# Performance work log

Measured on AMD Instinct MI355X. Metric: run time of the kernel, lower is better.

Reference implementation:

```python
import jax, jax.numpy as jnp
import numpy as np

NEG_SLOPE = 0.2
NUM_HEADS = 8
HEAD_DIM = 16


def setup_inputs() -> dict:
    key = jax.random.key(0)
    ks = jax.random.split(key, 14)
    n_nodes, n_edges = 50000, 800000
    in_f, out_f, e_f, H, D = 256, 128, 64, NUM_HEADS, HEAD_DIM
    s = lambda fan_in: 1.0 / np.sqrt(fan_in)
    return {
        "node_features": jax.random.normal(ks[0], (n_nodes, in_f), jnp.float32),
        "edge_index": jax.random.randint(ks[1], (2, n_edges), 0, n_nodes),
        "edge_features": jax.random.normal(ks[2], (n_edges, e_f), jnp.float32),
        "Wl": jax.random.normal(ks[3], (in_f, out_f), jnp.float32) * s(in_f),
        "bl": jnp.zeros((out_f,), jnp.float32),
        "Wr": jax.random.normal(ks[4], (in_f, out_f), jnp.float32) * s(in_f),
        "br": jnp.zeros((out_f,), jnp.float32),
        "We": jax.random.normal(ks[5], (e_f, H), jnp.float32) * s(e_f),
        "be": jnp.zeros((H,), jnp.float32),
        "attn_vector": jax.random.normal(ks[6], (H, D), jnp.float32) * 0.01,
        "Wv": jax.random.normal(ks[7], (in_f, out_f), jnp.float32) * s(in_f),
        "bv": jnp.zeros((out_f,), jnp.float32),
        "Wo": jax.random.normal(ks[8], (out_f, out_f), jnp.float32) * s(out_f),
        "bo": jnp.zeros((out_f,), jnp.float32),
    }


def reference(node_features, edge_index, edge_features,
              Wl, bl, Wr, br, We, be, attn_vector, Wv, bv, Wo, bo):
    n_nodes = node_features.shape[0]
    n_edges = edge_index.shape[1]
    H, D = attn_vector.shape
    sources, targets = edge_index[0], edge_index[1]

    # node projections: [N, H, D]
    left = (node_features @ Wl + bl).reshape(n_nodes, H, D)
    right = (node_features @ Wr + br).reshape(n_nodes, H, D)

    # per-edge GATv2 score: a^T LeakyReLU(W_l h_t + W_r h_s) + edge bias
    combined = left[targets] + right[sources]                      # [E, H, D]
    activated = jax.nn.leaky_relu(combined, negative_slope=NEG_SLOPE)
    attn_scores = jnp.einsum("ehd,hd->eh", activated, attn_vector)  # [E, H]
    attn_scores = attn_scores + (edge_features @ We + be)

    # segment softmax over incoming edges per target node
    max_scores = jax.ops.segment_max(attn_scores, targets, num_segments=n_nodes)
    attn_exp = jnp.exp(attn_scores - max_scores[targets])
    attn_sum = jax.ops.segment_sum(attn_exp, targets, num_segments=n_nodes) + 1e-10
    attn_probs = attn_exp / attn_sum[targets]                      # [E, H]

    # weighted scatter-aggregate of values
    values = (node_features @ Wv + bv).reshape(n_nodes, H, D)
    weighted = attn_probs[:, :, None] * values[sources]            # [E, H, D]
    aggregated = jax.ops.segment_sum(
        weighted.reshape(n_edges, H * D), targets, num_segments=n_nodes)
    return aggregated @ Wo + bo
```

## Files before the change

### kernel.cpp

```cpp
#include <hip/hip_runtime.h>
#include <hip/hip_bf16.h>
#include <stdint.h>

#define NUM_H 8
#define DIM 16
#define HD 128
#define IN_F 256
#define E_F 64
#define NEG_SLOPE 0.2f
#define NB 8
#define EB 32

#define NCT 24
#define KSTEPS 8
#define WELEMS (KSTEPS * NCT * 64 * 8)

typedef __bf16 bf16x8 __attribute__((ext_vector_type(8)));
typedef float f32x4 __attribute__((ext_vector_type(4)));
typedef short short8 __attribute__((ext_vector_type(8)));

__device__ __forceinline__ float b2f(__hip_bfloat16 x) { return __bfloat162float(x); }
__device__ __forceinline__ __hip_bfloat16 f2b(float x) { return __float2bfloat16(x); }
__device__ __forceinline__ float bs2f(short s) {
    uint32_t u = ((uint32_t)(uint16_t)s) << 16;
    return __builtin_bit_cast(float, u);
}

__global__ void k_zero_int(int* p, int n) {
    int i = blockIdx.x * blockDim.x + threadIdx.x;
    int stride = gridDim.x * blockDim.x;
    for (; i < n; i += stride) p[i] = 0;
}

__global__ void k_hist(const int* __restrict__ eidx, int* __restrict__ deg, int n_edges) {
    int e = blockIdx.x * blockDim.x + threadIdx.x;
    if (e < n_edges) atomicAdd(&deg[eidx[n_edges + e]], 1);
}

__global__ void k_scan(const int* __restrict__ deg, int* __restrict__ offs,
                       int* __restrict__ cursor, int n) {
    __shared__ int part[1024];
    int tid = threadIdx.x;
    int chunk = (n + 1023) / 1024;
    int base = tid * chunk;
    int hi = base + chunk < n ? base + chunk : n;
    int sum = 0;
    for (int i = base; i < hi; i++) sum += deg[i];
    part[tid] = sum;
    __syncthreads();
    for (int off = 1; off < 1024; off <<= 1) {
        int v = (tid >= off) ? part[tid - off] : 0;
        __syncthreads();
        part[tid] += v;
        __syncthreads();
    }
    int run = (tid == 0) ? 0 : part[tid - 1];
    for (int i = base; i < hi; i++) {
        offs[i] = run;
        cursor[i] = run;
        run += deg[i];
    }
    if (tid == 0) offs[n] = part[1023];
}

__global__ void k_scatter(const int* __restrict__ eidx, int* __restrict__ cursor,
                          int* __restrict__ eid, int n_edges) {
    int e = blockIdx.x * blockDim.x + threadIdx.x;
    if (e >= n_edges) return;
    int t = eidx[n_edges + e];
    int pos = atomicAdd(&cursor[t], 1);
    eid[pos] = e;
}

__global__ void k_wprep(const float* __restrict__ Wl, const float* __restrict__ Wr,
                        const float* __restrict__ Wv,
                        __bf16* __restrict__ Whi, __bf16* __restrict__ Wlo) {
    int tid = blockIdx.x * blockDim.x + threadIdx.x;
    if (tid >= KSTEPS * NCT * 64) return;
    int l = tid & 63;
    int ctks = tid >> 6;
    int ct = ctks % NCT;
    int ks = ctks / NCT;
    int gc = ct * 16 + (l & 15);
    int m = gc >> 7;
    int c = gc & 127;
    const float* W = (m == 0) ? Wl : (m == 1) ? Wr : Wv;
    bf16x8 h8, l8;
#pragma unroll
    for (int i = 0; i < 8; i++) {
        int k = ks * 32 + ((l >> 4) << 3) + i;
        float w = W[k * HD + c];
        __bf16 hi = (__bf16)w;
        __bf16 lo = (__bf16)(w - (float)hi);
        h8[i] = hi;
        l8[i] = lo;
    }
    *(bf16x8*)(Whi + (size_t)tid * 8) = h8;
    *(bf16x8*)(Wlo + (size_t)tid * 8) = l8;
}

__global__ __launch_bounds__(256, 2) void k_projm(
    const float* __restrict__ nf,
    const __bf16* __restrict__ Whi, const __bf16* __restrict__ Wlo,
    const float* __restrict__ bl, const float* __restrict__ br,
    const float* __restrict__ bv,
    __hip_bfloat16* __restrict__ left, __hip_bfloat16* __restrict__ right,
    __hip_bfloat16* __restrict__ val, int n_nodes) {
    int l = threadIdx.x & 63;
    int wave = threadIdx.x >> 6;
    int row0 = blockIdx.x * 64 + wave * 16;
    if (row0 >= n_nodes) return;
    int lr = l & 15, lg = l >> 4;
    const float* arow = nf + (size_t)(row0 + lr) * IN_F + lg * 8;

    const f32x4 zero = {0.f, 0.f, 0.f, 0.f};
    f32x4 acc[NCT];
#pragma unroll
    for (int ct = 0; ct < NCT; ct++) acc[ct] = zero;

    for (int ks = 0; ks < KSTEPS; ks++) {
        f32x4 a0 = *(const f32x4*)(arow + ks * 32);
        f32x4 a1 = *(const f32x4*)(arow + ks * 32 + 4);
        bf16x8 ah, al;
#pragma unroll
        for (int i = 0; i < 4; i++) {
            __bf16 h = (__bf16)a0[i];
            ah[i] = h;
            al[i] = (__bf16)(a0[i] - (float)h);
        }
#pragma unroll
        for (int i = 0; i < 4; i++) {
            __bf16 h = (__bf16)a1[i];
            ah[4 + i] = h;
            al[4 + i] = (__bf16)(a1[i] - (float)h);
        }
        const bf16x8* wh = (const bf16x8*)(Whi) + (size_t)ks * NCT * 64 + l;
        const bf16x8* wl = (const bf16x8*)(Wlo) + (size_t)ks * NCT * 64 + l;
#pragma unroll
        for (int ct = 0; ct < NCT; ct++) {
            bf16x8 bh = wh[ct * 64];
            bf16x8 blo = wl[ct * 64];
            acc[ct] = __builtin_amdgcn_mfma_f32_16x16x32_bf16(ah, bh, acc[ct], 0, 0, 0);
            acc[ct] = __builtin_amdgcn_mfma_f32_16x16x32_bf16(al, bh, acc[ct], 0, 0, 0);
            acc[ct] = __builtin_amdgcn_mfma_f32_16x16x32_bf16(ah, blo, acc[ct], 0, 0, 0);
        }
    }

#pragma unroll
    for (int ct = 0; ct < NCT; ct++) {
        const int m = ct >> 3;
        int c = ((ct & 7) << 4) + lr;
        float bias = (m == 0) ? bl[c] : (m == 1) ? br[c] : bv[c];
        __hip_bfloat16* dst = (m == 0) ? left : (m == 1) ? right : val;
#pragma unroll
        for (int r = 0; r < 4; r++) {
            int row = row0 + lg * 4 + r;
            dst[(size_t)row * HD + c] = f2b(acc[ct][r] + bias);
        }
    }
}

__global__ __launch_bounds__(256) void k_escore(
    const int* __restrict__ eidx, const float* __restrict__ ef,
    const float* __restrict__ We, const float* __restrict__ be,
    const float* __restrict__ av,
    const __hip_bfloat16* __restrict__ left,
    const __hip_bfloat16* __restrict__ right,
    __hip_bfloat16* __restrict__ es, int n_edges) {
    __shared__ float sef[EB][68];
    int tid = threadIdx.x;
    int e0 = blockIdx.x * EB;
    {
        const f32x4* src = (const f32x4*)(ef + (size_t)e0 * E_F);
        int lim = (n_edges - e0) * (E_F / 4);
        if (lim > EB * (E_F / 4)) lim = EB * (E_F / 4);
#pragma unroll 2
        for (int i = tid; i < lim; i += 256) {
            f32x4 v = src[i];
            int le = i >> 4;
            int k = (i & 15) << 2;
            *(f32x4*)&sef[le][k] = v;
        }
    }
    __syncthreads();
    int le = tid >> 3;
    int h = tid & 7;
    int e = e0 + le;
    if (e >= n_edges) return;
    int s = eidx[e];
    int t = eidx[n_edges + e];

    float sc = be[h];
    const float* row = &sef[le][0];
#pragma unroll
    for (int k4 = 0; k4 < E_F / 4; k4++) {
        f32x4 v = *(const f32x4*)(row + k4 * 4);
        sc += v[0] * We[(k4 * 4 + 0) * NUM_H + h] + v[1] * We[(k4 * 4 + 1) * NUM_H + h] +
              v[2] * We[(k4 * 4 + 2) * NUM_H + h] + v[3] * We[(k4 * 4 + 3) * NUM_H + h];
    }

    const short8* Lp = (const short8*)(left + (size_t)t * HD + h * DIM);
    const short8* Rp = (const short8*)(right + (size_t)s * HD + h * DIM);
    short8 l0 = Lp[0], l1 = Lp[1];
    short8 r0 = Rp[0], r1 = Rp[1];
    const float* avh = av + h * DIM;
#pragma unroll
    for (int d = 0; d < 8; d++) {
        float x = bs2f(l0[d]) + bs2f(r0[d]);
        x = x > 0.0f ? x : NEG_SLOPE * x;
        sc += x * avh[d];
    }
#pragma unroll
    for (int d = 0; d < 8; d++) {
        float x = bs2f(l1[d]) + bs2f(r1[d]);
        x = x > 0.0f ? x : NEG_SLOPE * x;
        sc += x * avh[8 + d];
    }
    es[(size_t)e * NUM_H + h] = f2b(expf(sc));
}

__global__ void k_agg(const int* __restrict__ offs, const int* __restrict__ eid,
                      const int* __restrict__ eidx,
                      const __hip_bfloat16* __restrict__ es,
                      const __hip_bfloat16* __restrict__ val,
                      float* __restrict__ nagg, int n_nodes) {
    int t = blockIdx.x;
    if (t >= n_nodes) return;
    int j = threadIdx.x;
    int h = j >> 4;
    int beg = offs[t], end = offs[t + 1];
    float acc = 0.0f, wsum = 0.0f;
    for (int i = beg; i < end; i++) {
        int e = eid[i];
        int s = eidx[e];
        float w = b2f(es[(size_t)e * NUM_H + h]);
        acc += w * b2f(val[(size_t)s * HD + j]);
        wsum += w;
    }
    nagg[(size_t)t * HD + j] = acc / (wsum + 1e-10f);
}

__global__ void k_out(const float* __restrict__ nagg, const float* __restrict__ Wo,
                      const float* __restrict__ bo, float* __restrict__ out, int n_nodes) {
    __shared__ float srow[NB][HD];
    int node0 = blockIdx.x * NB;
    int j = threadIdx.x;
    for (int i = j; i < NB * HD; i += 128)
        srow[i / HD][i % HD] = nagg[(size_t)node0 * HD + i];
    __syncthreads();
    float a[NB];
    float b = bo[j];
#pragma unroll
    for (int n = 0; n < NB; n++) a[n] = b;
    for (int k = 0; k < HD; k++) {
        float w = Wo[k * HD + j];
#pragma unroll
        for (int n = 0; n < NB; n++) a[n] += srow[n][k] * w;
    }
#pragma unroll
    for (int n = 0; n < NB; n++) out[(size_t)(node0 + n) * HD + j] = a[n];
}

extern "C" void kernel_launch(void* const* d_in, const int* in_sizes, int n_in,
                              void* d_out, int out_size, void* d_ws, size_t ws_size,
                              hipStream_t stream) {
    const float* nf = (const float*)d_in[0];
    const int* eidx = (const int*)d_in[1];
    const float* ef = (const float*)d_in[2];
    const float* Wl = (const float*)d_in[3];
    const float* bl = (const float*)d_in[4];
    const float* Wr = (const float*)d_in[5];
    const float* br = (const float*)d_in[6];
    const float* We = (const float*)d_in[7];
    const float* be = (const float*)d_in[8];
    const float* av = (const float*)d_in[9];
    const float* Wv = (const float*)d_in[10];
    const float* bv = (const float*)d_in[11];
    const float* Wo = (const float*)d_in[12];
    const float* bo = (const float*)d_in[13];
    float* out = (float*)d_out;

    const int n_nodes = in_sizes[0] / IN_F;
    const int n_edges = in_sizes[1] / 2;
    const size_t NHD = (size_t)n_nodes * HD;

    char* base = (char*)d_ws;
    __hip_bfloat16* left  = (__hip_bfloat16*)(base + 256);
    __hip_bfloat16* right = left + NHD;
    __hip_bfloat16* es    = right + NHD;
    int* deg    = (int*)(es + (size_t)n_edges * NUM_H);
    int* offs   = deg + n_nodes;
    int* cursor = offs + n_nodes + 1;
    int* eid    = cursor + n_nodes;
    __bf16* Whi = (__bf16*)es;
    __bf16* Wlo = Whi + (size_t)WELEMS;
    float* nagg = (float*)left;
    __hip_bfloat16* val = (__hip_bfloat16*)d_out;

    int eb = (n_edges + 255) / 256;

    k_wprep<<<(KSTEPS * NCT * 64 + 255) / 256, 256, 0, stream>>>(Wl, Wr, Wv, Whi, Wlo);

    k_zero_int<<<64, 256, 0, stream>>>(deg, n_nodes);
    k_hist<<<eb, 256, 0, stream>>>(eidx, deg, n_edges);
    k_scan<<<1, 1024, 0, stream>>>(deg, offs, cursor, n_nodes);
    k_scatter<<<eb, 256, 0, stream>>>(eidx, cursor, eid, n_edges);

    k_projm<<<(n_nodes + 63) / 64, 256, 0, stream>>>(nf, Whi, Wlo, bl, br, bv,
                                                     left, right, val, n_nodes);

    k_escore<<<(n_edges + EB - 1) / EB, 256, 0, stream>>>(
        eidx, ef, We, be, av, left, right, es, n_edges);

    k_agg<<<n_nodes, 128, 0, stream>>>(offs, eid, eidx, es, val, nagg, n_nodes);

    k_out<<<n_nodes / NB, 128, 0, stream>>>(nagg, Wo, bo, out, n_nodes);
}
```

Measured before the change: 860.7 us.

## Fuse CSR scatter into edge-score kernel and vectorize aggregation per wavefront

The separate scatter kernel is removed. The edge-score kernel now claims a CSR slot per edge with an atomic and writes the exp-score and source index directly in target-sorted order, so aggregation reads them contiguously instead of going through eid and eidx. The aggregation kernel now uses a single 64-lane wavefront per node: it processes four edges at once with 16-byte value loads, then reduces across sub-groups with shuffles. The trade-off is that atomic slot assignment makes the order of floating-point accumulation within each node nondeterministic.

```diff
diff --git a/kernel.cpp b/kernel.cpp
--- a/kernel.cpp
+++ b/kernel.cpp
@@ -63,15 +63,6 @@
     if (tid == 0) offs[n] = part[1023];
 }
 
-__global__ void k_scatter(const int* __restrict__ eidx, int* __restrict__ cursor,
-                          int* __restrict__ eid, int n_edges) {
-    int e = blockIdx.x * blockDim.x + threadIdx.x;
-    if (e >= n_edges) return;
-    int t = eidx[n_edges + e];
-    int pos = atomicAdd(&cursor[t], 1);
-    eid[pos] = e;
-}
-
 __global__ void k_wprep(const float* __restrict__ Wl, const float* __restrict__ Wr,
                         const float* __restrict__ Wv,
                         __bf16* __restrict__ Whi, __bf16* __restrict__ Wlo) {
@@ -166,7 +157,8 @@
     const float* __restrict__ av,
     const __hip_bfloat16* __restrict__ left,
     const __hip_bfloat16* __restrict__ right,
-    __hip_bfloat16* __restrict__ es, int n_edges) {
+    int* __restrict__ cursor, int* __restrict__ srcs,
+    __hip_bfloat16* __restrict__ es_csr, int n_edges) {
     __shared__ float sef[EB][68];
     int tid = threadIdx.x;
     int e0 = blockIdx.x * EB;
@@ -190,6 +182,11 @@
     int s = eidx[e];
     int t = eidx[n_edges + e];
 
+    int lane = tid & 63;
+    int pos = 0;
+    if (h == 0) pos = atomicAdd(&cursor[t], 1);
+    pos = __shfl(pos, lane & ~7);
+
     float sc = be[h];
     const float* row = &sef[le][0];
 #pragma unroll
@@ -216,28 +213,53 @@
         x = x > 0.0f ? x : NEG_SLOPE * x;
         sc += x * avh[8 + d];
     }
-    es[(size_t)e * NUM_H + h] = f2b(expf(sc));
-}
-
-__global__ void k_agg(const int* __restrict__ offs, const int* __restrict__ eid,
-                      const int* __restrict__ eidx,
-                      const __hip_bfloat16* __restrict__ es,
-                      const __hip_bfloat16* __restrict__ val,
-                      float* __restrict__ nagg, int n_nodes) {
+    if (h == 0) srcs[pos] = s;
+    es_csr[(size_t)pos * NUM_H + h] = f2b(expf(sc));
+}
+
+__global__ __launch_bounds__(64) void k_agg(
+    const int* __restrict__ offs, const int* __restrict__ srcs,
+    const __hip_bfloat16* __restrict__ es_csr,
+    const __hip_bfloat16* __restrict__ val,
+    float* __restrict__ nagg, int n_nodes) {
     int t = blockIdx.x;
     if (t >= n_nodes) return;
-    int j = threadIdx.x;
-    int h = j >> 4;
+    int lane = threadIdx.x;
+    int sub = lane >> 4;
+    int c16 = lane & 15;
+    int h = c16 >> 1;
     int beg = offs[t], end = offs[t + 1];
-    float acc = 0.0f, wsum = 0.0f;
-    for (int i = beg; i < end; i++) {
-        int e = eid[i];
-        int s = eidx[e];
-        float w = b2f(es[(size_t)e * NUM_H + h]);
-        acc += w * b2f(val[(size_t)s * HD + j]);
+
+    float acc[8] = {0.f, 0.f, 0.f, 0.f, 0.f, 0.f, 0.f, 0.f};
+    float wsum = 0.0f;
+#pragma unroll 2
+    for (int i0 = beg; i0 < end; i0 += 4) {
+        int i = i0 + sub;
+        bool act = i < end;
+        int ii = act ? i : beg;
+        int s = srcs[ii];
+        float w = b2f(es_csr[(size_t)ii * NUM_H + h]);
+        if (!act) w = 0.0f;
+        short8 v = *(const short8*)(val + (size_t)s * HD + c16 * 8);
         wsum += w;
-    }
-    nagg[(size_t)t * HD + j] = acc / (wsum + 1e-10f);
+#pragma unroll
+        for (int d = 0; d < 8; d++) acc[d] += w * bs2f(v[d]);
+    }
+#pragma unroll
+    for (int m = 16; m <= 32; m <<= 1) {
+        wsum += __shfl_xor(wsum, m);
+#pragma unroll
+        for (int d = 0; d < 8; d++) acc[d] += __shfl_xor(acc[d], m);
+    }
+    if (sub == 0) {
+        float inv = 1.0f / (wsum + 1e-10f);
+        f32x4 o0, o1;
+#pragma unroll
+        for (int d = 0; d < 4; d++) { o0[d] = acc[d] * inv; o1[d] = acc[4 + d] * inv; }
+        float* dst = nagg + (size_t)t * HD + c16 * 8;
+        *(f32x4*)dst = o0;
+        *(f32x4*)(dst + 4) = o1;
+    }
 }
 
 __global__ void k_out(const float* __restrict__ nagg, const float* __restrict__ Wo,
@@ -287,12 +309,12 @@
     char* base = (char*)d_ws;
     __hip_bfloat16* left  = (__hip_bfloat16*)(base + 256);
     __hip_bfloat16* right = left + NHD;
-    __hip_bfloat16* es    = right + NHD;
-    int* deg    = (int*)(es + (size_t)n_edges * NUM_H);
+    __hip_bfloat16* es_csr = right + NHD;
+    int* deg    = (int*)(es_csr + (size_t)n_edges * NUM_H);
     int* offs   = deg + n_nodes;
     int* cursor = offs + n_nodes + 1;
-    int* eid    = cursor + n_nodes;
-    __bf16* Whi = (__bf16*)es;
+    int* srcs   = cursor + n_nodes;
+    __bf16* Whi = (__bf16*)es_csr;
     __bf16* Wlo = Whi + (size_t)WELEMS;
     float* nagg = (float*)left;
     __hip_bfloat16* val = (__hip_bfloat16*)d_out;
@@ -304,15 +326,14 @@
     k_zero_int<<<64, 256, 0, stream>>>(deg, n_nodes);
     k_hist<<<eb, 256, 0, stream>>>(eidx, deg, n_edges);
     k_scan<<<1, 1024, 0, stream>>>(deg, offs, cursor, n_nodes);
-    k_scatter<<<eb, 256, 0, stream>>>(eidx, cursor, eid, n_edges);
 
     k_projm<<<(n_nodes + 63) / 64, 256, 0, stream>>>(nf, Whi, Wlo, bl, br, bv,
                                                      left, right, val, n_nodes);
 
     k_escore<<<(n_edges + EB - 1) / EB, 256, 0, stream>>>(
-        eidx, ef, We, be, av, left, right, es, n_edges);
-
-    k_agg<<<n_nodes, 128, 0, stream>>>(offs, eid, eidx, es, val, nagg, n_nodes);
+        eidx, ef, We, be, av, left, right, cursor, srcs, es_csr, n_edges);
+
+    k_agg<<<n_nodes, 64, 0, stream>>>(offs, srcs, es_csr, val, nagg, n_nodes);
 
     k_out<<<n_nodes / NB, 128, 0, stream>>>(nagg, Wo, bo, out, n_nodes);
 }
```

After: 779.9 us. 1.1x faster.
